# Performance work log

Measured on AMD Instinct MI355X. Metric: run time of the kernel, lower is better.

## Reference

```python
import jax, jax.numpy as jnp
import numpy as np

NEG_INF = -1.0e9  # masked_fill value used by the torch module
LN_EPS = 1e-6


def setup_inputs() -> dict:
    key = jax.random.key(0)
    ks = jax.random.split(key, 10)
    B, S, D = 4, 1024, 1024
    H, DK, DV = 16, 64, 64
    q = jax.random.normal(ks[0], (B, S, D), dtype=jnp.float32)
    k = jax.random.normal(ks[1], (B, S, D), dtype=jnp.float32)
    v = jax.random.normal(ks[2], (B, S, D), dtype=jnp.float32)
    mask = jax.random.randint(ks[3], (B, S, S), 0, 2, dtype=jnp.int32)
    sc = 1.0 / np.sqrt(D)
    wq = jax.random.normal(ks[4], (H, D, DK), dtype=jnp.float32) * sc  # per-head W_qs stacked
    wk = jax.random.normal(ks[5], (H, D, DK), dtype=jnp.float32) * sc
    wv = jax.random.normal(ks[6], (H, D, DV), dtype=jnp.float32) * sc
    fc_w = jax.random.normal(ks[7], (D, H * DV), dtype=jnp.float32) * (1.0 / np.sqrt(H * DV))  # torch Linear weight [out,in]
    ln_g = jnp.ones((D,), dtype=jnp.float32)
    ln_b = jnp.zeros((D,), dtype=jnp.float32)
    return {"q": q, "k": k, "v": v, "mask": mask, "wq": wq, "wk": wk,
            "wv": wv, "fc_w": fc_w, "ln_g": ln_g, "ln_b": ln_b}


def reference(q, k, v, mask, wq, wk, wv, fc_w, ln_g, ln_b):
    # Batched equivalent of the per-head Python loop (dropout in eval mode = identity).
    B, S, D = q.shape
    H, _, DK = wq.shape
    DV = wv.shape[-1]
    temperature = jnp.asarray(DK, q.dtype) ** 0.5
    residual = q
    qh = jnp.einsum('bqd,hdk->bhqk', q, wq)   # [B,H,Q,DK]
    kh = jnp.einsum('bsd,hdk->bhsk', k, wk)   # [B,H,K,DK]
    vh = jnp.einsum('bsd,hdv->bhsv', v, wv)   # [B,H,K,DV]
    attn = jnp.einsum('bhqe,bhke->bhqk', qh / temperature, kh)  # [B,H,Q,K]
    attn = jnp.where(mask[:, None, :, :] == 0, jnp.asarray(NEG_INF, attn.dtype), attn)
    attn = jax.nn.softmax(attn, axis=-1)
    heads = jnp.einsum('bhqk,bhkv->bhqv', attn, vh)             # [B,H,Q,DV]
    # concat heads along feature dim in head order (matches torch.cat of the loop outputs)
    concat = jnp.transpose(heads, (0, 2, 1, 3)).reshape(B, S, H * DV)
    out = concat @ fc_w.T                                        # fc, no bias
    out = out + residual
    mu = jnp.mean(out, axis=-1, keepdims=True)
    var = jnp.mean(jnp.square(out - mu), axis=-1, keepdims=True)
    out = (out - mu) / jnp.sqrt(var + LN_EPS) * ln_g + ln_b
    return out
```

## Files before the change

kernel.cpp:

```cpp
#include <hip/hip_runtime.h>
#include <hip/hip_bf16.h>

typedef __bf16 bf16x8 __attribute__((ext_vector_type(8)));
typedef __bf16 bf16x4 __attribute__((ext_vector_type(4)));
typedef __bf16 bf16x2 __attribute__((ext_vector_type(2)));
typedef float f32x4 __attribute__((ext_vector_type(4)));
typedef unsigned int u32x2 __attribute__((ext_vector_type(2)));

#define MFMA16(a, b, c) __builtin_amdgcn_mfma_f32_16x16x32_bf16(a, b, c, 0, 0, 0)

static constexpr int M_ = 4096;

__device__ __forceinline__ void gload_lds16(const void* g, void* l) {
  __builtin_amdgcn_global_load_lds((const __attribute__((address_space(1))) void*)g,
                                   (__attribute__((address_space(3))) void*)l, 16, 0, 0);
}

__device__ __forceinline__ float exp2_hw(float x) {
  float r;
  asm("v_exp_f32 %0, %1" : "=v"(r) : "v"(x));
  return r;
}

#define SWZ(rowv, c16) (((rowv) * 64) + (((c16) ^ ((rowv) & 7)) * 8))

__global__ __launch_bounds__(256) void prep(const float* __restrict__ q,
                                            const float* __restrict__ k,
                                            const float* __restrict__ v,
                                            const float* __restrict__ fc_w,
                                            const float* __restrict__ wq,
                                            const float* __restrict__ wk,
                                            const float* __restrict__ wv,
                                            const int* __restrict__ mask,
                                            __bf16* __restrict__ QKVBF,
                                            __bf16* __restrict__ WFC,
                                            __bf16* __restrict__ W3T,
                                            unsigned long long* __restrict__ bits) {
  __shared__ float tile[64][65];
  int bx = blockIdx.x;
  const int t = threadIdx.x;

  if (bx < 6144) {
    const int z = bx >> 11;
    const float* src = z == 0 ? q : (z == 1 ? k : v);
    __bf16* dst = QKVBF + (size_t)z * 4194304;
    int i = (bx & 2047) * 256 + t;
    const float4* p = (const float4*)src + (size_t)i * 2;
    float4 a = p[0], b = p[1];
    bf16x8 o;
    o[0] = (__bf16)a.x; o[1] = (__bf16)a.y; o[2] = (__bf16)a.z; o[3] = (__bf16)a.w;
    o[4] = (__bf16)b.x; o[5] = (__bf16)b.y; o[6] = (__bf16)b.z; o[7] = (__bf16)b.w;
    *((bf16x8*)dst + i) = o;
    return;
  }
  bx -= 6144;
  if (bx < 512) {
    int i = bx * 256 + t;
    const float4* p = (const float4*)fc_w + (size_t)i * 2;
    float4 a = p[0], b = p[1];
    bf16x8 o;
    o[0] = (__bf16)a.x; o[1] = (__bf16)a.y; o[2] = (__bf16)a.z; o[3] = (__bf16)a.w;
    o[4] = (__bf16)b.x; o[5] = (__bf16)b.y; o[6] = (__bf16)b.z; o[7] = (__bf16)b.w;
    *((bf16x8*)WFC + i) = o;
    return;
  }
  bx -= 512;
  if (bx < 768) {
    const int z = bx >> 8, rem = bx & 255;
    const float* w = z == 0 ? wq : (z == 1 ? wk : wv);
    const float scale = z == 0 ? 0.125f * 1.4426950408889634f : 1.0f;
    __bf16* o = W3T + (size_t)z * 1048576;
    const int h = rem & 15, d0 = (rem >> 4) * 64;
    const int r = t >> 2, c0 = (t & 3) * 16;
    const float4* s4 = (const float4*)(w + ((size_t)h * 1024 + d0 + r) * 64 + c0);
#pragma unroll
    for (int j = 0; j < 4; ++j) {
      float4 vv = s4[j];
      tile[r][c0 + 4 * j + 0] = vv.x; tile[r][c0 + 4 * j + 1] = vv.y;
      tile[r][c0 + 4 * j + 2] = vv.z; tile[r][c0 + 4 * j + 3] = vv.w;
    }
    __syncthreads();
    __bf16* dst = o + ((size_t)(h * 64 + r)) * 1024 + d0 + c0;
    bf16x8 o0, o1;
#pragma unroll
    for (int j = 0; j < 8; ++j) o0[j] = (__bf16)(tile[c0 + j][r] * scale);
#pragma unroll
    for (int j = 0; j < 8; ++j) o1[j] = (__bf16)(tile[c0 + 8 + j][r] * scale);
    *(bf16x8*)dst = o0;
    *(bf16x8*)(dst + 8) = o1;
    return;
  }
  bx -= 768;
  {
    const int wid = bx * 4 + (t >> 6);
    const int lane = t & 63;
#pragma unroll
    for (int i = 0; i < 16; ++i) {
      int widx = wid * 16 + i;
      int qrow = widx & 1023;
      int bkt = widx >> 10;
      int b = bkt >> 4, kt = bkt & 15;
      int mval = mask[((size_t)b * 1024 + qrow) * 1024 + kt * 64 + lane];
      unsigned long long bal = __ballot(mval != 0);
      if (lane == 0) bits[widx] = bal;
    }
  }
}

__global__ __launch_bounds__(256) void gemm_qkv(const __bf16* __restrict__ Abase,
                                                const __bf16* __restrict__ Btbase,
                                                __bf16* __restrict__ HEADS) {
  __shared__ __bf16 SMEM[8448];
  const int L = blockIdx.x;
  const int wl = (L & 7) * 96 + (L >> 3);
  const int bn = wl & 7;
  const int bmz = wl >> 3;
  const int bm = bmz & 31, z = bmz >> 5;
  const __bf16* A = Abase + (size_t)z * 4194304;
  const __bf16* Bt = Btbase + (size_t)z * 1048576;
  const int tid = threadIdx.x, lane = tid & 63;
  const int w = tid >> 6;
  const int wr = (w >> 1) * 64, wc = (w & 1) * 64;
  const int lr = lane & 15, lh = lane >> 4;

  f32x4 acc[4][4];
#pragma unroll
  for (int m = 0; m < 4; ++m)
#pragma unroll
    for (int n = 0; n < 4; ++n) {
      f32x4 zz = {0.f, 0.f, 0.f, 0.f};
      acc[m][n] = zz;
    }

  for (int kt = 0; kt < 32; ++kt) {
#pragma unroll
    for (int i = 0; i < 2; ++i) {
      int o = i * 4096 + tid * 16;
      int row = o >> 6, cb = o & 63;
      gload_lds16((const char*)A + (((size_t)(bm * 128 + row)) * 1024 + kt * 32) * 2 + cb,
                  (char*)SMEM + o);
      gload_lds16((const char*)Bt + (((size_t)(bn * 128 + row)) * 1024 + kt * 32) * 2 + cb,
                  (char*)SMEM + 8192 + o);
    }
    __syncthreads();
    bf16x8 af[4], bfr[4];
#pragma unroll
    for (int m = 0; m < 4; ++m) af[m] = *(const bf16x8*)&SMEM[(wr + m * 16 + lr) * 32 + lh * 8];
#pragma unroll
    for (int n = 0; n < 4; ++n)
      bfr[n] = *(const bf16x8*)&SMEM[4096 + (wc + n * 16 + lr) * 32 + lh * 8];
#pragma unroll
    for (int m = 0; m < 4; ++m)
#pragma unroll
      for (int n = 0; n < 4; ++n) acc[m][n] = MFMA16(af[m], bfr[n], acc[m][n]);
    __syncthreads();
  }

  if (z == 2) {
    const int hl = w & 1;
    const size_t vtbase = 2ull * 4194304;
    const size_t bb = (size_t)(bm >> 3) * 16 + bn * 2;
    const int kkbase = (bm & 7) * 128;
#pragma unroll
    for (int p = 0; p < 2; ++p) {
      if (hl == p) {
#pragma unroll
        for (int m = 0; m < 4; ++m)
#pragma unroll
          for (int n = 0; n < 4; ++n) {
            const int dk = n * 16 + lr;
            const int s = wr + m * 16 + lh * 4;
            bf16x4 pv;
#pragma unroll
            for (int j = 0; j < 4; ++j) pv[j] = (__bf16)acc[m][n][j];
            *(bf16x4*)&SMEM[dk * 132 + s] = pv;
          }
      }
      __syncthreads();
      {
        const int dk = tid >> 2, sc = tid & 3;
        const __bf16* srcp = &SMEM[dk * 132 + sc * 32];
        __bf16* dstp = HEADS + vtbase + ((bb + p) * 64 + dk) * 1024 + kkbase + sc * 32;
#pragma unroll
        for (int u = 0; u < 8; ++u) *(bf16x4*)(dstp + u * 4) = *(const bf16x4*)(srcp + u * 4);
      }
      __syncthreads();
    }
    return;
  }

#pragma unroll
  for (int p = 0; p < 2; ++p) {
    if ((w >> 1) == p) {
#pragma unroll
      for (int m = 0; m < 4; ++m)
#pragma unroll
        for (int n = 0; n < 4; ++n)
#pragma unroll
          for (int reg = 0; reg < 4; ++reg)
            SMEM[(m * 16 + lh * 4 + reg) * 132 + wc + n * 16 + lr] = (__bf16)acc[m][n][reg];
    }
    __syncthreads();
    {
      const int rowl = tid >> 2, c0 = (tid & 3) * 32;
      const int row = bm * 128 + p * 64 + rowl;
      const int b = row >> 10, s = row & 1023;
      const int h = bn * 2 + (c0 >> 6), dk0 = c0 & 63;
      __bf16* dst = HEADS + (size_t)z * 4194304 + (((size_t)b * 16 + h) * 1024 + s) * 64 + dk0;
      const __bf16* srcp = &SMEM[rowl * 132 + c0];
#pragma unroll
      for (int u = 0; u < 8; ++u) *(bf16x4*)(dst + u * 4) = *(const bf16x4*)(srcp + u * 4);
    }
    __syncthreads();
  }
}

__global__ __launch_bounds__(256) void gemm_fc64(const __bf16* __restrict__ A,
                                                 const __bf16* __restrict__ Bt,
                                                 float* __restrict__ O,
                                                 const float* __restrict__ resid) {
  __shared__ __bf16 As[64 * 32];
  __shared__ __bf16 Bs[128 * 32];
  const int L = blockIdx.x;
  const int wl = (L & 7) * 64 + (L >> 3);
  const int bn = wl & 7, bm = wl >> 3;
  const int tid = threadIdx.x, lane = tid & 63;
  const int w = tid >> 6;
  const int wc = w * 32;
  const int lr = lane & 15, lh = lane >> 4;

  f32x4 acc[4][2];
#pragma unroll
  for (int m = 0; m < 4; ++m)
#pragma unroll
    for (int n = 0; n < 2; ++n) {
      f32x4 z = {0.f, 0.f, 0.f, 0.f};
      acc[m][n] = z;
    }

  for (int kt = 0; kt < 32; ++kt) {
    {
      int o = tid * 16;
      int row = o >> 6, cb = o & 63;
      gload_lds16((const char*)A + (((size_t)(bm * 64 + row)) * 1024 + kt * 32) * 2 + cb,
                  (char*)As + o);
    }
#pragma unroll
    for (int i = 0; i < 2; ++i) {
      int o = i * 4096 + tid * 16;
      int row = o >> 6, cb = o & 63;
      gload_lds16((const char*)Bt + (((size_t)(bn * 128 + row)) * 1024 + kt * 32) * 2 + cb,
                  (char*)Bs + o);
    }
    __syncthreads();
    bf16x8 af[4], bfr[2];
#pragma unroll
    for (int m = 0; m < 4; ++m) af[m] = *(const bf16x8*)&As[(m * 16 + lr) * 32 + lh * 8];
#pragma unroll
    for (int n = 0; n < 2; ++n) bfr[n] = *(const bf16x8*)&Bs[(wc + n * 16 + lr) * 32 + lh * 8];
#pragma unroll
    for (int m = 0; m < 4; ++m)
#pragma unroll
      for (int n = 0; n < 2; ++n) acc[m][n] = MFMA16(af[m], bfr[n], acc[m][n]);
    __syncthreads();
  }

#pragma unroll
  for (int m = 0; m < 4; ++m)
#pragma unroll
    for (int n = 0; n < 2; ++n)
#pragma unroll
      for (int reg = 0; reg < 4; ++reg) {
        int row = bm * 64 + m * 16 + lh * 4 + reg;
        int col = bn * 128 + wc + n * 16 + lr;
        size_t idx = (size_t)row * 1024 + col;
        O[idx] = acc[m][n][reg] + resid[idx];
      }
}

__global__ __launch_bounds__(256, 4) void attn_kernel(const __bf16* __restrict__ HEADS,
                                                      const unsigned long long* __restrict__ m64,
                                                      __bf16* __restrict__ concat) {
  const __bf16* QH = HEADS;
  const __bf16* KH = HEADS + (size_t)M_ * 1024;
  const __bf16* VT = HEADS + (size_t)2 * M_ * 1024;
  __shared__ __bf16 Ks[2][2][32 * 64];
  __shared__ __bf16 Vs[2][2][64 * 32];
  __shared__ unsigned Psw[2][4][256];

  const int d = blockIdx.x;
  const int xcd = d & 7, j = d >> 3;
  const int grp = xcd * 8 + (j >> 4);
  const int qt = j & 15;
  const int h = grp & 15, b = grp >> 4;

  const int tid = threadIdx.x, lane = tid & 63, w = tid >> 6;
  const int lr = lane & 15, lh = lane >> 4;
  const size_t headoff = ((size_t)b * 16 + h) * 65536;
  const char* Kbase = (const char*)(KH + headoff);
  const char* Vbase = (const char*)(VT + headoff);

  const int krow = tid >> 3, kg = tid & 7;
  const int kgo = krow * 128 + ((kg ^ (krow & 7)) * 16);
  const int vrow = tid >> 2, vg = tid & 3;
  const int vgo = vrow * 2048 + ((vg ^ ((vrow >> 1) & 3)) * 16);
  const int ldsb = tid * 16;

  const char* kpA = Kbase + kgo;
  const char* kpB = Kbase + 65536 + kgo;
  const char* vpA = Vbase + vgo;
  const char* vpB = Vbase + 1024 + vgo;

#define STAGE(buf)                                          \
  do {                                                      \
    gload_lds16(kpA, (char*)Ks[buf][0] + ldsb);             \
    gload_lds16(kpB, (char*)Ks[buf][1] + ldsb);             \
    gload_lds16(vpA, (char*)Vs[buf][0] + ldsb);             \
    gload_lds16(vpB, (char*)Vs[buf][1] + ldsb);             \
    kpA += 4096; kpB += 4096; vpA += 64; vpB += 64;         \
  } while (0)

  const int qrow = qt * 64 + w * 16 + lr;
  bf16x8 qa[2];
  {
    const __bf16* qptr = QH + headoff + (size_t)qrow * 64 + lh * 8;
    qa[0] = *(const bf16x8*)qptr;
    qa[1] = *(const bf16x8*)(qptr + 32);
  }
  f32x4 oacc[4];
#pragma unroll
  for (int g = 0; g < 4; ++g) {
    f32x4 z = {0.f, 0.f, 0.f, 0.f};
    oacc[g] = z;
  }
  float lrun = 0.f;

  const unsigned long long* m64A = m64 + (size_t)b * 16384 + qrow;
  const unsigned long long* m64B = m64A + 8192;
  unsigned long long pairA = m64A[0], pairB = m64B[0];
  unsigned long long pairAn = 0, pairBn = 0;

  const int vcol = (lh ^ ((lr >> 1) & 3)) * 8;
  const int pread = lr * 32 + vcol;
  const int pG = (lr >> 1) & 3;
  int kread[2][2], vread[4];
#pragma unroll
  for (int n = 0; n < 2; ++n)
#pragma unroll
    for (int h2 = 0; h2 < 2; ++h2) kread[n][h2] = SWZ(n * 16 + lr, h2 * 4 + lh);
#pragma unroll
  for (int g = 0; g < 4; ++g) vread[g] = (g * 16 + lr) * 32 + vcol;

  STAGE(0);
  __syncthreads();

#pragma unroll 2
  for (int t = 0; t < 16; ++t) {
    const int cur = t & 1;
    if ((t & 1) == 0 && t < 14) {
      pairAn = m64A[((t >> 1) + 1) * 1024];
      pairBn = m64B[((t >> 1) + 1) * 1024];
    }
    const unsigned mwA = (t & 1) ? (unsigned)(pairA >> 32) : (unsigned)pairA;
    const unsigned mwB = (t & 1) ? (unsigned)(pairB >> 32) : (unsigned)pairB;
    if (t < 15) STAGE(cur ^ 1);

    f32x4 sA[2], sB[2];
#pragma unroll
    for (int n = 0; n < 2; ++n) {
      f32x4 z = {0.f, 0.f, 0.f, 0.f};
      sA[n] = z; sB[n] = z;
    }
    __builtin_amdgcn_s_setprio(1);
#pragma unroll
    for (int n = 0; n < 2; ++n)
#pragma unroll
      for (int h2 = 0; h2 < 2; ++h2) {
        bf16x8 kbA = *(const bf16x8*)&Ks[cur][0][kread[n][h2]];
        bf16x8 kbB = *(const bf16x8*)&Ks[cur][1][kread[n][h2]];
        sA[n] = MFMA16(kbA, qa[h2], sA[n]);
        sB[n] = MFMA16(kbB, qa[h2], sB[n]);
      }
    __builtin_amdgcn_s_setprio(0);

#pragma unroll
    for (int n = 0; n < 2; ++n)
#pragma unroll
      for (int r = 0; r < 4; ++r) {
        unsigned bit = (mwA >> (n * 16 + lh * 4 + r)) & 1u;
        float p = bit ? exp2_hw(sA[n][r]) : 0.0f;
        sA[n][r] = p;
        lrun += p;
      }
#pragma unroll
    for (int n = 0; n < 2; ++n)
#pragma unroll
      for (int r = 0; r < 4; ++r) {
        unsigned bit = (mwB >> (n * 16 + lh * 4 + r)) & 1u;
        float p = bit ? exp2_hw(sB[n][r]) : 0.0f;
        sB[n][r] = p;
        lrun += p;
      }

#pragma unroll
    for (int n = 0; n < 2; ++n) {
      bf16x2 p0, p1;
      p0[0] = (__bf16)sA[n][0]; p0[1] = (__bf16)sA[n][1];
      p1[0] = (__bf16)sA[n][2]; p1[1] = (__bf16)sA[n][3];
      int G = n * 2 + (lh >> 1);
      int addr = lr * 16 + ((G ^ pG) * 4) + (lh & 1) * 2;
      u32x2 wv;
      wv[0] = __builtin_bit_cast(unsigned, p0);
      wv[1] = __builtin_bit_cast(unsigned, p1);
      *(u32x2*)&Psw[0][w][addr] = wv;
    }
#pragma unroll
    for (int n = 0; n < 2; ++n) {
      bf16x2 p0, p1;
      p0[0] = (__bf16)sB[n][0]; p0[1] = (__bf16)sB[n][1];
      p1[0] = (__bf16)sB[n][2]; p1[1] = (__bf16)sB[n][3];
      int G = n * 2 + (lh >> 1);
      int addr = lr * 16 + ((G ^ pG) * 4) + (lh & 1) * 2;
      u32x2 wv;
      wv[0] = __builtin_bit_cast(unsigned, p0);
      wv[1] = __builtin_bit_cast(unsigned, p1);
      *(u32x2*)&Psw[1][w][addr] = wv;
    }
    bf16x8 paA = *(const bf16x8*)&((const __bf16*)Psw[0][w])[pread];
    bf16x8 paB = *(const bf16x8*)&((const __bf16*)Psw[1][w])[pread];

    __builtin_amdgcn_s_setprio(1);
#pragma unroll
    for (int g = 0; g < 4; ++g) {
      bf16x8 vbA = *(const bf16x8*)&Vs[cur][0][vread[g]];
      bf16x8 vbB = *(const bf16x8*)&Vs[cur][1][vread[g]];
      oacc[g] = MFMA16(paA, vbA, oacc[g]);
      oacc[g] = MFMA16(paB, vbB, oacc[g]);
    }
    __builtin_amdgcn_s_setprio(0);
    if (t & 1) { pairA = pairAn; pairB = pairBn; }
    __syncthreads();
  }
#undef STAGE

  lrun += __shfl_xor(lrun, 16, 64);
  lrun += __shfl_xor(lrun, 32, 64);
  const float linv = 1.0f / (lrun + 1e-30f);
  const int qg0 = qt * 64 + w * 16 + lh * 4;
#pragma unroll
  for (int r = 0; r < 4; ++r) {
    const float ir = __shfl(linv, (lane & 48) | (lh * 4 + r), 64);
#pragma unroll
    for (int g = 0; g < 4; ++g)
      concat[((size_t)b * 1024 + qg0 + r) * 1024 + h * 64 + g * 16 + lr] =
          (__bf16)(oacc[g][r] * ir);
  }
}

__global__ __launch_bounds__(256) void ln_kernel(const float* __restrict__ in,
                                                 const float* __restrict__ gam,
                                                 const float* __restrict__ bet,
                                                 float* __restrict__ out) {
  const int row = blockIdx.x, t = threadIdx.x;
  const float4* x4 = (const float4*)(in + (size_t)row * 1024);
  float4 v = x4[t];
  float s = v.x + v.y + v.z + v.w;
  float sq = v.x * v.x + v.y * v.y + v.z * v.z + v.w * v.w;
#pragma unroll
  for (int off = 1; off < 64; off <<= 1) {
    s += __shfl_xor(s, off, 64);
    sq += __shfl_xor(sq, off, 64);
  }
  __shared__ float red[8];
  const int w = t >> 6, lane = t & 63;
  if (lane == 0) { red[w] = s; red[4 + w] = sq; }
  __syncthreads();
  s = red[0] + red[1] + red[2] + red[3];
  sq = red[4] + red[5] + red[6] + red[7];
  const float mu = s * (1.0f / 1024.0f);
  const float var = sq * (1.0f / 1024.0f) - mu * mu;
  const float rstd = rsqrtf(var + 1e-6f);
  float4 g4 = ((const float4*)gam)[t];
  float4 b4 = ((const float4*)bet)[t];
  float4 o;
  o.x = (v.x - mu) * rstd * g4.x + b4.x;
  o.y = (v.y - mu) * rstd * g4.y + b4.y;
  o.z = (v.z - mu) * rstd * g4.z + b4.z;
  o.w = (v.w - mu) * rstd * g4.w + b4.w;
  ((float4*)(out + (size_t)row * 1024))[t] = o;
}

extern "C" void kernel_launch(void* const* d_in, const int* in_sizes, int n_in,
                              void* d_out, int out_size, void* d_ws, size_t ws_size,
                              hipStream_t stream) {
  (void)in_sizes; (void)n_in; (void)out_size; (void)ws_size;
  const float* q = (const float*)d_in[0];
  const float* k = (const float*)d_in[1];
  const float* v = (const float*)d_in[2];
  const int* mask = (const int*)d_in[3];
  const float* wq = (const float*)d_in[4];
  const float* wk = (const float*)d_in[5];
  const float* wv = (const float*)d_in[6];
  const float* fc_w = (const float*)d_in[7];
  const float* ln_g = (const float*)d_in[8];
  const float* ln_b = (const float*)d_in[9];
  float* out = (float*)d_out;

  __bf16* QKVBF = (__bf16*)d_ws;
  __bf16* W3T   = QKVBF + 3ull * 4194304;
  __bf16* WFC   = W3T + 3ull * 1048576;
  __bf16* HEADS = WFC + 1048576;
  __bf16* CONCAT = HEADS + 3ull * 4194304;
  float* OUT1 = (float*)(CONCAT + 4194304);
  unsigned long long* MASKB = (unsigned long long*)OUT1;

  prep<<<8448, 256, 0, stream>>>(q, k, v, fc_w, wq, wk, wv, mask, QKVBF, WFC, W3T, MASKB);
  gemm_qkv<<<768, 256, 0, stream>>>(QKVBF, W3T, HEADS);
  attn_kernel<<<1024, 256, 0, stream>>>(HEADS, MASKB, CONCAT);
  gemm_fc64<<<512, 256, 0, stream>>>(CONCAT, WFC, OUT1, q);
  ln_kernel<<<4096, 256, 0, stream>>>(OUT1, ln_g, ln_b, out);
}
```

Measured before the change: 118.7 us.

## Double-buffer LDS tiles in QKV and FC GEMMs with async prefetch

Both GEMM kernels now keep two LDS stages. The next K-tile is issued with global_load_lds before the MFMAs on the current tile run, and the loop needs one barrier per iteration instead of two. Address pointers are precomputed and bumped each step, and the MFMA block is wrapped in s_setprio. The aim is to hide global load latency behind compute, at the cost of doubling LDS use per block, which may lower occupancy.

```diff
diff --git a/kernel.cpp b/kernel.cpp
--- a/kernel.cpp
+++ b/kernel.cpp
@@ -110,7 +110,7 @@
 __global__ __launch_bounds__(256) void gemm_qkv(const __bf16* __restrict__ Abase,
                                                 const __bf16* __restrict__ Btbase,
                                                 __bf16* __restrict__ HEADS) {
-  __shared__ __bf16 SMEM[8448];
+  __shared__ __bf16 SMEM[16384];
   const int L = blockIdx.x;
   const int wl = (L & 7) * 96 + (L >> 3);
   const int bn = wl & 7;
@@ -123,6 +123,24 @@
   const int wr = (w >> 1) * 64, wc = (w & 1) * 64;
   const int lr = lane & 15, lh = lane >> 4;
 
+  const int o0 = tid * 16;
+  const int row0 = o0 >> 6, cb = o0 & 63;
+  const char* apA0 = (const char*)A + ((size_t)(bm * 128 + row0) * 1024) * 2 + cb;
+  const char* apA1 = apA0 + 64 * 2048;
+  const char* apB0 = (const char*)Bt + ((size_t)(bn * 128 + row0) * 1024) * 2 + cb;
+  const char* apB1 = apB0 + 64 * 2048;
+  char* smem = (char*)SMEM;
+
+#define QSTAGE(buf)                                         \
+  do {                                                      \
+    char* dd = smem + (buf) * 16384;                        \
+    gload_lds16(apA0, dd + o0);                             \
+    gload_lds16(apA1, dd + 4096 + o0);                      \
+    gload_lds16(apB0, dd + 8192 + o0);                      \
+    gload_lds16(apB1, dd + 12288 + o0);                     \
+    apA0 += 64; apA1 += 64; apB0 += 64; apB1 += 64;         \
+  } while (0)
+
   f32x4 acc[4][4];
 #pragma unroll
   for (int m = 0; m < 4; ++m)
@@ -132,29 +150,29 @@
       acc[m][n] = zz;
     }
 
+  QSTAGE(0);
+  __syncthreads();
+
   for (int kt = 0; kt < 32; ++kt) {
-#pragma unroll
-    for (int i = 0; i < 2; ++i) {
-      int o = i * 4096 + tid * 16;
-      int row = o >> 6, cb = o & 63;
-      gload_lds16((const char*)A + (((size_t)(bm * 128 + row)) * 1024 + kt * 32) * 2 + cb,
-                  (char*)SMEM + o);
-      gload_lds16((const char*)Bt + (((size_t)(bn * 128 + row)) * 1024 + kt * 32) * 2 + cb,
-                  (char*)SMEM + 8192 + o);
-    }
+    const int cur = kt & 1;
+    if (kt < 31) QSTAGE(cur ^ 1);
+    const int abase = cur * 8192;
+    bf16x8 af[4], bfr[4];
+#pragma unroll
+    for (int m = 0; m < 4; ++m)
+      af[m] = *(const bf16x8*)&SMEM[abase + (wr + m * 16 + lr) * 32 + lh * 8];
+#pragma unroll
+    for (int n = 0; n < 4; ++n)
+      bfr[n] = *(const bf16x8*)&SMEM[abase + 4096 + (wc + n * 16 + lr) * 32 + lh * 8];
+    __builtin_amdgcn_s_setprio(1);
+#pragma unroll
+    for (int m = 0; m < 4; ++m)
+#pragma unroll
+      for (int n = 0; n < 4; ++n) acc[m][n] = MFMA16(af[m], bfr[n], acc[m][n]);
+    __builtin_amdgcn_s_setprio(0);
     __syncthreads();
-    bf16x8 af[4], bfr[4];
-#pragma unroll
-    for (int m = 0; m < 4; ++m) af[m] = *(const bf16x8*)&SMEM[(wr + m * 16 + lr) * 32 + lh * 8];
-#pragma unroll
-    for (int n = 0; n < 4; ++n)
-      bfr[n] = *(const bf16x8*)&SMEM[4096 + (wc + n * 16 + lr) * 32 + lh * 8];
-#pragma unroll
-    for (int m = 0; m < 4; ++m)
-#pragma unroll
-      for (int n = 0; n < 4; ++n) acc[m][n] = MFMA16(af[m], bfr[n], acc[m][n]);
-    __syncthreads();
-  }
+  }
+#undef QSTAGE
 
   if (z == 2) {
     const int hl = w & 1;
@@ -219,8 +237,7 @@
                                                  const __bf16* __restrict__ Bt,
                                                  float* __restrict__ O,
                                                  const float* __restrict__ resid) {
-  __shared__ __bf16 As[64 * 32];
-  __shared__ __bf16 Bs[128 * 32];
+  __shared__ __bf16 SMEM[12288];
   const int L = blockIdx.x;
   const int wl = (L & 7) * 64 + (L >> 3);
   const int bn = wl & 7, bm = wl >> 3;
@@ -229,6 +246,22 @@
   const int wc = w * 32;
   const int lr = lane & 15, lh = lane >> 4;
 
+  const int o0 = tid * 16;
+  const int row0 = o0 >> 6, cb = o0 & 63;
+  const char* apA = (const char*)A + ((size_t)(bm * 64 + row0) * 1024) * 2 + cb;
+  const char* apB0 = (const char*)Bt + ((size_t)(bn * 128 + row0) * 1024) * 2 + cb;
+  const char* apB1 = apB0 + 64 * 2048;
+  char* smem = (char*)SMEM;
+
+#define FSTAGE(buf)                                         \
+  do {                                                      \
+    gload_lds16(apA, smem + (buf) * 4096 + o0);             \
+    char* dd = smem + 8192 + (buf) * 8192;                  \
+    gload_lds16(apB0, dd + o0);                             \
+    gload_lds16(apB1, dd + 4096 + o0);                      \
+    apA += 64; apB0 += 64; apB1 += 64;                      \
+  } while (0)
+
   f32x4 acc[4][2];
 #pragma unroll
   for (int m = 0; m < 4; ++m)
@@ -238,32 +271,29 @@
       acc[m][n] = z;
     }
 
+  FSTAGE(0);
+  __syncthreads();
+
   for (int kt = 0; kt < 32; ++kt) {
-    {
-      int o = tid * 16;
-      int row = o >> 6, cb = o & 63;
-      gload_lds16((const char*)A + (((size_t)(bm * 64 + row)) * 1024 + kt * 32) * 2 + cb,
-                  (char*)As + o);
-    }
-#pragma unroll
-    for (int i = 0; i < 2; ++i) {
-      int o = i * 4096 + tid * 16;
-      int row = o >> 6, cb = o & 63;
-      gload_lds16((const char*)Bt + (((size_t)(bn * 128 + row)) * 1024 + kt * 32) * 2 + cb,
-                  (char*)Bs + o);
-    }
+    const int cur = kt & 1;
+    if (kt < 31) FSTAGE(cur ^ 1);
+    const int ab = cur * 2048;
+    const int bb = 4096 + cur * 4096;
+    bf16x8 af[4], bfr[2];
+#pragma unroll
+    for (int m = 0; m < 4; ++m) af[m] = *(const bf16x8*)&SMEM[ab + (m * 16 + lr) * 32 + lh * 8];
+#pragma unroll
+    for (int n = 0; n < 2; ++n)
+      bfr[n] = *(const bf16x8*)&SMEM[bb + (wc + n * 16 + lr) * 32 + lh * 8];
+    __builtin_amdgcn_s_setprio(1);
+#pragma unroll
+    for (int m = 0; m < 4; ++m)
+#pragma unroll
+      for (int n = 0; n < 2; ++n) acc[m][n] = MFMA16(af[m], bfr[n], acc[m][n]);
+    __builtin_amdgcn_s_setprio(0);
     __syncthreads();
-    bf16x8 af[4], bfr[2];
-#pragma unroll
-    for (int m = 0; m < 4; ++m) af[m] = *(const bf16x8*)&As[(m * 16 + lr) * 32 + lh * 8];
-#pragma unroll
-    for (int n = 0; n < 2; ++n) bfr[n] = *(const bf16x8*)&Bs[(wc + n * 16 + lr) * 32 + lh * 8];
-#pragma unroll
-    for (int m = 0; m < 4; ++m)
-#pragma unroll
-      for (int n = 0; n < 2; ++n) acc[m][n] = MFMA16(af[m], bfr[n], acc[m][n]);
-    __syncthreads();
-  }
+  }
+#undef FSTAGE
 
 #pragma unroll
   for (int m = 0; m < 4; ++m)
```

After: 119.7 us. About the same (+0.9%).
